# Optimization experiments

Measured on AMD Instinct MI355X. Metric: run time of the kernel, lower is better.

Reference implementation:

```python
import jax, jax.numpy as jnp
import numpy as np
from jax import lax

D_MODEL = 512
N_LAYERS = 12
D_STATE = 16
D_INNER = 2 * D_MODEL          # expand=2
DT_RANK = D_MODEL // 16        # 32
D_CONV = 4
L = 361                        # 19x19 Go board
B = 64


def silu(v):
    return v * jax.nn.sigmoid(v)


def setup_inputs() -> dict:
    key = jax.random.key(0)
    ks = jax.random.split(key, 24)
    s = 0.02
    inp = {
        "x": jax.random.normal(ks[0], (B, 17, 19, 19), dtype=jnp.float32),
        "conv1_w": jax.random.normal(ks[1], (D_MODEL // 4, 17, 3, 3)) * s,
        "conv1_b": jnp.zeros((D_MODEL // 4,)),
        "conv2_w": jax.random.normal(ks[2], (D_MODEL, D_MODEL // 4, 1, 1)) * s,
        "conv2_b": jnp.zeros((D_MODEL,)),
        "spatial_link": jax.random.normal(ks[3], (L, D_MODEL)) * s,
        # stacked per-layer Mamba parameters (leading dim = N_LAYERS)
        "in_proj_w": jax.random.normal(ks[4], (N_LAYERS, 2 * D_INNER, D_MODEL)) * s,
        "conv1d_w": jax.random.normal(ks[5], (N_LAYERS, D_INNER, D_CONV)) * 0.1,
        "conv1d_b": jnp.zeros((N_LAYERS, D_INNER)),
        "x_proj_w": jax.random.normal(ks[6], (N_LAYERS, DT_RANK + 2 * D_STATE, D_INNER)) * s,
        "dt_proj_w": jax.random.normal(ks[7], (N_LAYERS, D_INNER, DT_RANK)) * 0.1,
        "dt_proj_b": jax.random.uniform(ks[8], (N_LAYERS, D_INNER), minval=-4.0, maxval=-2.0),
        "A_log": jnp.broadcast_to(jnp.log(jnp.arange(1.0, D_STATE + 1.0)), (N_LAYERS, D_INNER, D_STATE)) * jnp.ones((N_LAYERS, D_INNER, 1)),
        "D_skip": jnp.ones((N_LAYERS, D_INNER)),
        "out_proj_w": jax.random.normal(ks[9], (N_LAYERS, D_MODEL, D_INNER)) * s,
        "ln_g": jnp.ones((D_MODEL,)),
        "ln_b": jnp.zeros((D_MODEL,)),
        "policy_w": jax.random.normal(ks[10], (362, D_MODEL)) * s,
        "policy_b": jnp.zeros((362,)),
        "value_w": jax.random.normal(ks[11], (1, D_MODEL)) * s,
        "value_b": jnp.zeros((1,)),
    }
    return inp


def _mamba_block(u, p):
    """One Mamba block. u: [B, L, d_model]; p: per-layer params."""
    ipw, cw, cb, xpw, dpw, dpb, alog, dsk, opw = p
    Lh = u.shape[1]
    xz = jnp.einsum('bld,ed->ble', u, ipw)           # [B,L,2*d_inner]
    xc, z = jnp.split(xz, 2, axis=-1)
    # depthwise causal conv1d (kernel 4, left pad 3)
    xp = jnp.pad(xc, ((0, 0), (D_CONV - 1, 0), (0, 0)))
    xc = sum(xp[:, k:k + Lh, :] * cw[:, k] for k in range(D_CONV)) + cb
    xc = silu(xc)
    dbc = jnp.einsum('bld,ed->ble', xc, xpw)          # [B,L,dt_rank+2N]
    dt_r = dbc[..., :DT_RANK]
    Bc = dbc[..., DT_RANK:DT_RANK + D_STATE]
    Cc = dbc[..., DT_RANK + D_STATE:]
    dt = jax.nn.softplus(jnp.einsum('blr,dr->bld', dt_r, dpw) + dpb)  # [B,L,d_inner]
    A = -jnp.exp(alog)                                # [d_inner, N]

    def step(h, xs_t):
        dt_t, B_t, C_t, u_t = xs_t                    # [B,d_inner],[B,N],[B,N],[B,d_inner]
        dA = jnp.exp(dt_t[:, :, None] * A)            # [B,d_inner,N]
        h = dA * h + (dt_t * u_t)[:, :, None] * B_t[:, None, :]
        y = jnp.einsum('bdn,bn->bd', h, C_t)
        return h, y

    h0 = jnp.zeros((u.shape[0], D_INNER, D_STATE), dtype=u.dtype)
    xs = (dt.transpose(1, 0, 2), Bc.transpose(1, 0, 2),
          Cc.transpose(1, 0, 2), xc.transpose(1, 0, 2))
    _, ys = lax.scan(step, h0, xs)                    # ys: [L,B,d_inner]
    y = ys.transpose(1, 0, 2) + xc * dsk
    y = y * silu(z)
    return jnp.einsum('bld,ed->ble', y, opw)


def reference(x, conv1_w, conv1_b, conv2_w, conv2_b, spatial_link,
              in_proj_w, conv1d_w, conv1d_b, x_proj_w, dt_proj_w, dt_proj_b,
              A_log, D_skip, out_proj_w, ln_g, ln_b,
              policy_w, policy_b, value_w, value_b):
    dn = ('NCHW', 'OIHW', 'NCHW')
    h = lax.conv_general_dilated(x, conv1_w, (1, 1), 'SAME', dimension_numbers=dn)
    h = silu(h + conv1_b[None, :, None, None])
    h = lax.conv_general_dilated(h, conv2_w, (1, 1), 'SAME', dimension_numbers=dn)
    h = h + conv2_b[None, :, None, None]
    b = h.shape[0]
    u = h.reshape(b, D_MODEL, L).transpose(0, 2, 1) + spatial_link  # [B,L,d_model]

    def layer(carry, p):
        return carry + _mamba_block(carry, p), None

    u, _ = lax.scan(layer, u, (in_proj_w, conv1d_w, conv1d_b, x_proj_w,
                               dt_proj_w, dt_proj_b, A_log, D_skip, out_proj_w))

    mu = u.mean(-1, keepdims=True)
    var = ((u - mu) ** 2).mean(-1, keepdims=True)
    un = (u - mu) / jnp.sqrt(var + 1e-5) * ln_g + ln_b
    xg = un.mean(axis=1)                               # [B,d_model]
    policy = xg @ policy_w.T + policy_b                # [B,362]
    value = jnp.tanh(xg @ value_w.T + value_b)         # [B,1]
    return policy, value
```

## Files before the change

kernel.cpp:

```cpp
#include <hip/hip_runtime.h>
#include <hip/hip_bf16.h>
#include <cstdint>

typedef unsigned int  uint32;
typedef unsigned short u16;
typedef __attribute__((ext_vector_type(8))) __bf16  bf16x8;
typedef __attribute__((ext_vector_type(4))) float   f32x4;
typedef __attribute__((ext_vector_type(4))) uint32  u32x4;
typedef __attribute__((ext_vector_type(4))) u16     u16x4;

constexpr int BB = 64;
constexpr int LL = 361;
constexpr int DM = 512;
constexpr int DI = 1024;
constexpr int MM = BB * LL;
constexpr int MP = 23168;
constexpr int POL_OUT = BB * 362;

constexpr size_t SCRATCH_BYTES = 700ull * 1024 * 1024;
__device__ __attribute__((aligned(256))) char g_scratch[SCRATCH_BYTES];

__device__ __forceinline__ uint32 bf_rne(float x) {
  uint32 u = __float_as_uint(x);
  return (u + 0x7FFFu + ((u >> 16) & 1u)) >> 16;
}
__device__ __forceinline__ void split2(float v, u16& h, u16& l) {
  uint32 b = __float_as_uint(v);
  h = (u16)(b >> 16);
  l = (u16)bf_rne(v - __uint_as_float(b & 0xFFFF0000u));
}
__device__ __forceinline__ float join2(u16 h, u16 l) {
  return __uint_as_float((uint32)h << 16) + __uint_as_float((uint32)l << 16);
}

template<int ROWS>
__device__ __forceinline__ void stage_swz(const u16* __restrict__ plane, int row0,
                                          int K, int k0, u16* lds,
                                          int wave, int lane) {
  const int lrow = lane >> 3, lslot = lane & 7;
  constexpr int RPW = ROWS / 4;
#pragma unroll
  for (int i = 0; i < RPW / 8; ++i) {
    int rr = wave * RPW + i * 8 + lrow;
    int sg = lslot ^ (rr & 7);
    const u16* src = plane + (size_t)(row0 + rr) * K + k0 + sg * 8;
    u16* dst = lds + (wave * RPW + i * 8) * 64;
    __builtin_amdgcn_global_load_lds(
        (const __attribute__((address_space(1))) void*)src,
        (__attribute__((address_space(3))) void*)dst, 16, 0, 0);
  }
}

template<int BM, int BN, bool RES, bool WPL>
__global__ __launch_bounds__(256, 2) void gemm_pl(
    const u16* __restrict__ Ahi, const u16* __restrict__ Alo,
    const u16* __restrict__ Whi, const u16* __restrict__ Wlo,
    float* __restrict__ C, u16* __restrict__ Chi, u16* __restrict__ Clo,
    int M, int K, int ldc)
{
  constexpr int BK = 64;
  __shared__ __attribute__((aligned(16))) u16 sAh[BM * 64];
  __shared__ __attribute__((aligned(16))) u16 sAl[BM * 64];
  __shared__ __attribute__((aligned(16))) u16 sWh[BN * 64];
  __shared__ __attribute__((aligned(16))) u16 sWl[BN * 64];
  const int tid = threadIdx.x;
  const int m0 = blockIdx.x * BM;
  const int n0 = blockIdx.y * BN;
  const int wave = tid >> 6, lane = tid & 63;
  const int wm = (wave >> 1) * (BM / 2);
  const int wn = (wave & 1) * (BN / 2);
  constexpr int FM = BM / 32, FN = BN / 32;
  f32x4 acc[FM][FN];
#pragma unroll
  for (int i = 0; i < FM; ++i)
#pragma unroll
    for (int j = 0; j < FN; ++j) acc[i][j] = f32x4{0.f, 0.f, 0.f, 0.f};
  const int lr = lane & 15, lq = lane >> 4;

  for (int k0 = 0; k0 < K; k0 += BK) {
    __syncthreads();
    stage_swz<BM>(Ahi, m0, K, k0, sAh, wave, lane);
    stage_swz<BM>(Alo, m0, K, k0, sAl, wave, lane);
    stage_swz<BN>(Whi, n0, K, k0, sWh, wave, lane);
    stage_swz<BN>(Wlo, n0, K, k0, sWl, wave, lane);
    __syncthreads();
#pragma unroll
    for (int kk = 0; kk < 2; ++kk) {
      bf16x8 ah[FM], al[FM], bh[FN], bl[FN];
#pragma unroll
      for (int f = 0; f < FM; ++f) {
        int row = wm + f * 16 + lr;
        int off = row * 128 + (((kk * 4 + lq) ^ (row & 7)) << 4);
        ah[f] = *(const bf16x8*)((const char*)sAh + off);
        al[f] = *(const bf16x8*)((const char*)sAl + off);
      }
#pragma unroll
      for (int f = 0; f < FN; ++f) {
        int row = wn + f * 16 + lr;
        int off = row * 128 + (((kk * 4 + lq) ^ (row & 7)) << 4);
        bh[f] = *(const bf16x8*)((const char*)sWh + off);
        bl[f] = *(const bf16x8*)((const char*)sWl + off);
      }
#pragma unroll
      for (int i = 0; i < FM; ++i)
#pragma unroll
        for (int j = 0; j < FN; ++j) {
          acc[i][j] = __builtin_amdgcn_mfma_f32_16x16x32_bf16(ah[i], bh[j], acc[i][j], 0, 0, 0);
          acc[i][j] = __builtin_amdgcn_mfma_f32_16x16x32_bf16(ah[i], bl[j], acc[i][j], 0, 0, 0);
          acc[i][j] = __builtin_amdgcn_mfma_f32_16x16x32_bf16(al[i], bh[j], acc[i][j], 0, 0, 0);
        }
    }
  }
#pragma unroll
  for (int i = 0; i < FM; ++i)
#pragma unroll
    for (int j = 0; j < FN; ++j) {
      int col = n0 + wn + j * 16 + lr;
#pragma unroll
      for (int q = 0; q < 4; ++q) {
        int row = m0 + wm + i * 16 + lq * 4 + q;
        if (row < M) {
          size_t idx = (size_t)row * ldc + col;
          float v = acc[i][j][q];
          if (RES) v += C[idx];
          C[idx] = v;
          if (WPL) { u16 h, l; split2(v, h, l); Chi[idx] = h; Clo[idx] = l; }
        }
      }
    }
}

__global__ void wconv_kernel(const float* __restrict__ w, u16* __restrict__ hi,
                             u16* __restrict__ lo, int n4) {
  int i = blockIdx.x * 256 + threadIdx.x;
  if (i >= n4) return;
  f32x4 v = *(const f32x4*)&w[(size_t)i * 4];
  u16x4 hv, lv;
#pragma unroll
  for (int q = 0; q < 4; ++q) { u16 h, l; split2(v[q], h, l); hv[q] = h; lv[q] = l; }
  *(u16x4*)&hi[(size_t)i * 4] = hv;
  *(u16x4*)&lo[(size_t)i * 4] = lv;
}

__global__ void w2t_kernel(const float* __restrict__ w2, float* __restrict__ w2t) {
  int i = blockIdx.x * 256 + threadIdx.x;
  if (i < 512 * 128) { int co = i >> 7, ci = i & 127; w2t[ci * 512 + co] = w2[i]; }
}

__global__ void pwt_kernel(const float* __restrict__ pw, float* __restrict__ pwt) {
  int i = blockIdx.x * 256 + threadIdx.x;
  if (i < 362 * 512) { int j = i / 512, dd = i & 511; pwt[dd * 362 + j] = pw[i]; }
}

__global__ void conv1_kernel(const float* __restrict__ x, const float* __restrict__ w,
                             const float* __restrict__ bias, float* __restrict__ h1) {
  __shared__ float xs[17 * 361];
  __shared__ float wls[16 * 153];
  const int b = blockIdx.x, cg = blockIdx.y * 16;
  const int tid = threadIdx.x;
  for (int i = tid; i < 17 * 361; i += 384) xs[i] = x[(size_t)b * 17 * 361 + i];
  for (int i = tid; i < 16 * 153; i += 384) wls[i] = w[(size_t)cg * 153 + i];
  __syncthreads();
  if (tid >= 361) return;
  const int py = tid / 19, px = tid % 19;
  float* outp = h1 + ((size_t)b * 361 + tid) * 128 + cg;
  for (int c = 0; c < 16; ++c) {
    float acc = bias[cg + c];
    const float* wc = wls + c * 153;
    for (int ci = 0; ci < 17; ++ci) {
      const float* xi = xs + ci * 361;
      const float* wi = wc + ci * 9;
#pragma unroll
      for (int ky = 0; ky < 3; ++ky) {
        int iy = py + ky - 1;
        if (iy < 0 || iy >= 19) continue;
#pragma unroll
        for (int kx = 0; kx < 3; ++kx) {
          int ix = px + kx - 1;
          if (ix < 0 || ix >= 19) continue;
          acc += xi[iy * 19 + ix] * wi[ky * 3 + kx];
        }
      }
    }
    outp[c] = acc / (1.f + __expf(-acc));
  }
}

__global__ void conv2_kernel(const float* __restrict__ h1, const float* __restrict__ w2t,
                             const float* __restrict__ b2, const float* __restrict__ sl,
                             float* __restrict__ u, u16* __restrict__ uhi,
                             u16* __restrict__ ulo) {
  __shared__ float hs[8][128];
  const int b = blockIdx.x, l0 = blockIdx.y * 8;
  const int nl = min(8, 361 - l0);
  const int tid = threadIdx.x;
  for (int i = tid; i < nl * 128; i += 512)
    hs[i >> 7][i & 127] = h1[((size_t)b * 361 + l0 + (i >> 7)) * 128 + (i & 127)];
  __syncthreads();
  float acc[8];
#pragma unroll
  for (int j = 0; j < 8; ++j) acc[j] = 0.f;
  for (int ci = 0; ci < 128; ++ci) {
    float wv = w2t[ci * 512 + tid];
#pragma unroll
    for (int j = 0; j < 8; ++j) acc[j] += hs[j][ci] * wv;
  }
  float bb = b2[tid];
  for (int j = 0; j < nl; ++j) {
    int l = l0 + j;
    size_t idx = ((size_t)b * 361 + l) * 512 + tid;
    float v = acc[j] + bb + sl[(size_t)l * 512 + tid];
    u[idx] = v;
    u16 h, lo; split2(v, h, lo);
    uhi[idx] = h; ulo[idx] = lo;
  }
}

__global__ void conv1d_kernel(const float* __restrict__ xz, const float* __restrict__ cw,
                              const float* __restrict__ cb, u16* __restrict__ xchi,
                              u16* __restrict__ xclo) {
  const int b = blockIdx.x, l0 = blockIdx.y * 32;
  const int d = threadIdx.x * 4;
  float w[4][4], bias[4];
#pragma unroll
  for (int j = 0; j < 4; ++j) {
#pragma unroll
    for (int k = 0; k < 4; ++k) w[j][k] = cw[(d + j) * 4 + k];
    bias[j] = cb[d + j];
  }
  f32x4 h0 = {0, 0, 0, 0}, h1v = {0, 0, 0, 0}, h2v = {0, 0, 0, 0};
  if (l0 >= 3) h0  = *(const f32x4*)&xz[((size_t)b * 361 + l0 - 3) * 2048 + d];
  if (l0 >= 2) h1v = *(const f32x4*)&xz[((size_t)b * 361 + l0 - 2) * 2048 + d];
  if (l0 >= 1) h2v = *(const f32x4*)&xz[((size_t)b * 361 + l0 - 1) * 2048 + d];
  const int nl = min(32, 361 - l0);
  for (int t = 0; t < nl; ++t) {
    const int l = l0 + t;
    f32x4 cur = *(const f32x4*)&xz[((size_t)b * 361 + l) * 2048 + d];
    u16x4 hv, lv;
#pragma unroll
    for (int j = 0; j < 4; ++j) {
      float v = h0[j] * w[j][0] + h1v[j] * w[j][1] + h2v[j] * w[j][2] + cur[j] * w[j][3] + bias[j];
      v = v / (1.f + __expf(-v));
      u16 h, lo; split2(v, h, lo); hv[j] = h; lv[j] = lo;
    }
    size_t idx = ((size_t)b * 361 + l) * 1024 + d;
    *(u16x4*)&xchi[idx] = hv;
    *(u16x4*)&xclo[idx] = lv;
    h0 = h1v; h1v = h2v; h2v = cur;
  }
}

__global__ void dt_kernel(const float* __restrict__ dbc, const float* __restrict__ dpw,
                          const float* __restrict__ dpb, float* __restrict__ dty) {
  __shared__ float dbs[32][32];
  const int m0 = blockIdx.x * 32, d0 = blockIdx.y * 256;
  const int tid = threadIdx.x;
  {
    int r = tid >> 3, c = (tid & 7) * 4;
    *(f32x4*)&dbs[r][c] = *(const f32x4*)&dbc[(size_t)(m0 + r) * 64 + c];
  }
  __syncthreads();
  float wreg[32];
  const float* wp = dpw + (size_t)(d0 + tid) * 32;
#pragma unroll
  for (int q = 0; q < 8; ++q) {
    f32x4 v = *(const f32x4*)&wp[q * 4];
    wreg[q * 4] = v[0]; wreg[q * 4 + 1] = v[1]; wreg[q * 4 + 2] = v[2]; wreg[q * 4 + 3] = v[3];
  }
  const float bias = dpb[d0 + tid];
  for (int m = 0; m < 32; ++m) {
    float acc = bias;
#pragma unroll
    for (int r = 0; r < 32; ++r) acc += dbs[m][r] * wreg[r];
    float sp = fmaxf(acc, 0.f) + log1pf(__expf(-fabsf(acc)));
    dty[(size_t)(m0 + m) * 1024 + d0 + tid] = sp;
  }
}

__global__ void scan_kernel(const float* __restrict__ dbc, const u16* __restrict__ xchi,
                            const u16* __restrict__ xclo, const float* __restrict__ xz,
                            const float* __restrict__ alog, const float* __restrict__ dsk,
                            const float* __restrict__ dty, u16* __restrict__ yhi,
                            u16* __restrict__ ylo) {
  const int b = blockIdx.x;
  const int d = blockIdx.y * 256 + threadIdx.x;
  float Ax[16], h[16];
#pragma unroll
  for (int n = 0; n < 16; ++n) { Ax[n] = -__expf(alog[(size_t)d * 16 + n]); h[n] = 0.f; }
  const float dval = dsk[d];
  const size_t mb = (size_t)b * 361;
  for (int t = 0; t < 361; ++t) {
    const size_t m = mb + t;
    const float dtv = dty[m * 1024 + d];
    const float uv  = join2(xchi[m * 1024 + d], xclo[m * 1024 + d]);
    const float zv  = xz[m * 2048 + 1024 + d];
    const float* bcp = dbc + m * 64 + 32;
    const float du = dtv * uv;
    float yv = 0.f;
#pragma unroll
    for (int n = 0; n < 16; ++n) {
      float dA = __expf(dtv * Ax[n]);
      h[n] = dA * h[n] + du * bcp[n];
      yv += h[n] * bcp[16 + n];
    }
    yv += uv * dval;
    float sz = zv / (1.f + __expf(-zv));
    float yo = yv * sz;
    u16 hh, ll; split2(yo, hh, ll);
    yhi[m * 1024 + d] = hh;
    ylo[m * 1024 + d] = ll;
  }
}

__global__ void ln_stats_kernel(const float* __restrict__ u, float* __restrict__ muv,
                                float* __restrict__ rsd) {
  const int m = blockIdx.x * 4 + (threadIdx.x >> 6);
  const int lane = threadIdx.x & 63;
  const float* row = u + (size_t)m * 512;
  float s = 0.f, s2 = 0.f;
#pragma unroll
  for (int i = 0; i < 2; ++i) {
    f32x4 v = *(const f32x4*)&row[(lane + i * 64) * 4];
    s  += v[0] + v[1] + v[2] + v[3];
    s2 += v[0] * v[0] + v[1] * v[1] + v[2] * v[2] + v[3] * v[3];
  }
#pragma unroll
  for (int o = 32; o > 0; o >>= 1) { s += __shfl_down(s, o); s2 += __shfl_down(s2, o); }
  if (lane == 0) {
    float mean = s * (1.f / 512.f);
    float var = s2 * (1.f / 512.f) - mean * mean;
    muv[m] = mean;
    rsd[m] = rsqrtf(var + 1e-5f);
  }
}

__global__ void xg_kernel(const float* __restrict__ u, const float* __restrict__ muv,
                          const float* __restrict__ rsd, const float* __restrict__ g,
                          const float* __restrict__ bta, float* __restrict__ xg) {
  const int b = blockIdx.x, dd = threadIdx.x;
  float acc = 0.f;
  const size_t mb = (size_t)b * 361;
  for (int l = 0; l < 361; ++l) {
    const size_t m = mb + l;
    acc += (u[m * 512 + dd] - muv[m]) * rsd[m];
  }
  xg[(size_t)b * 512 + dd] = g[dd] * acc * (1.f / 361.f) + bta[dd];
}

__global__ void head_kernel(const float* __restrict__ xg, const float* __restrict__ pwt,
                            const float* __restrict__ pb, const float* __restrict__ vw,
                            const float* __restrict__ vb, float* __restrict__ out) {
  __shared__ float xs[512];
  const int b = blockIdx.x, tid = threadIdx.x;
  xs[tid] = xg[(size_t)b * 512 + tid];
  __syncthreads();
  if (tid < 362) {
    float acc = pb[tid];
    for (int dd = 0; dd < 512; ++dd) acc += xs[dd] * pwt[dd * 362 + tid];
    out[(size_t)b * 362 + tid] = acc;
  } else if (tid == 384) {
    float acc = vb[0];
    for (int dd = 0; dd < 512; ++dd) acc += xs[dd] * vw[dd];
    out[POL_OUT + b] = tanhf(acc);
  }
}

extern "C" void kernel_launch(void* const* d_in, const int* in_sizes, int n_in,
                              void* d_out, int out_size, void* d_ws, size_t ws_size,
                              hipStream_t stream) {
  const float* x     = (const float*)d_in[0];
  const float* c1w   = (const float*)d_in[1];
  const float* c1b   = (const float*)d_in[2];
  const float* c2w   = (const float*)d_in[3];
  const float* c2b   = (const float*)d_in[4];
  const float* slink = (const float*)d_in[5];
  const float* ipw   = (const float*)d_in[6];
  const float* cdw   = (const float*)d_in[7];
  const float* cdb   = (const float*)d_in[8];
  const float* xpw   = (const float*)d_in[9];
  const float* dpw   = (const float*)d_in[10];
  const float* dpb   = (const float*)d_in[11];
  const float* alog  = (const float*)d_in[12];
  const float* dskp  = (const float*)d_in[13];
  const float* opw   = (const float*)d_in[14];
  const float* lng   = (const float*)d_in[15];
  const float* lnb   = (const float*)d_in[16];
  const float* pw    = (const float*)d_in[17];
  const float* pb    = (const float*)d_in[18];
  const float* vw    = (const float*)d_in[19];
  const float* vb    = (const float*)d_in[20];
  float* out = (float*)d_out;
  (void)in_sizes; (void)n_in; (void)out_size; (void)d_ws; (void)ws_size;

  char* base = nullptr;
  hipGetSymbolAddress((void**)&base, HIP_SYMBOL(g_scratch));
  size_t off = 0;
  auto carve = [&](size_t bytes) -> char* {
    char* p = base + off;
    off += (bytes + 255) & ~(size_t)255;
    return p;
  };
  float* u    = (float*)carve((size_t)MM * DM * 4);
  float* xz   = (float*)carve((size_t)MM * 2 * DI * 4);
  float* dty  = (float*)carve((size_t)MM * DI * 4);
  float* dbc  = (float*)carve((size_t)MM * 64 * 4);
  float* h1   = (float*)carve((size_t)BB * LL * 128 * 4);
  float* w2t  = (float*)carve(512 * 128 * 4);
  float* pwt  = (float*)carve(512 * 362 * 4);
  float* muv  = (float*)carve((size_t)MM * 4);
  float* rsd  = (float*)carve((size_t)MM * 4);
  float* xg   = (float*)carve((size_t)BB * DM * 4);
  u16* uhi  = (u16*)carve((size_t)MP * DM * 2);
  u16* ulo  = (u16*)carve((size_t)MP * DM * 2);
  u16* xchi = (u16*)carve((size_t)MP * DI * 2);
  u16* xclo = (u16*)carve((size_t)MP * DI * 2);
  u16* yhi  = (u16*)carve((size_t)MP * DI * 2);
  u16* ylo  = (u16*)carve((size_t)MP * DI * 2);
  u16* wih = (u16*)carve((size_t)12 * 2048 * 512 * 2);
  u16* wil = (u16*)carve((size_t)12 * 2048 * 512 * 2);
  u16* wxh = (u16*)carve((size_t)12 * 64 * 1024 * 2);
  u16* wxl = (u16*)carve((size_t)12 * 64 * 1024 * 2);
  u16* woh = (u16*)carve((size_t)12 * 512 * 1024 * 2);
  u16* wol = (u16*)carve((size_t)12 * 512 * 1024 * 2);

  wconv_kernel<<<dim3(12288), dim3(256), 0, stream>>>(ipw, wih, wil, 3145728);
  wconv_kernel<<<dim3(768),   dim3(256), 0, stream>>>(xpw, wxh, wxl, 196608);
  wconv_kernel<<<dim3(6144),  dim3(256), 0, stream>>>(opw, woh, wol, 1572864);
  w2t_kernel<<<dim3(256), dim3(256), 0, stream>>>(c2w, w2t);
  pwt_kernel<<<dim3(724), dim3(256), 0, stream>>>(pw, pwt);

  conv1_kernel<<<dim3(64, 8),  dim3(384), 0, stream>>>(x, c1w, c1b, h1);
  conv2_kernel<<<dim3(64, 46), dim3(512), 0, stream>>>(h1, w2t, c2b, slink, u, uhi, ulo);

  for (int layer = 0; layer < 12; ++layer) {
    gemm_pl<128, 128, false, false><<<dim3(181, 16), dim3(256), 0, stream>>>(
        uhi, ulo, wih + (size_t)layer * 1048576, wil + (size_t)layer * 1048576,
        xz, nullptr, nullptr, MM, 512, 2048);
    conv1d_kernel<<<dim3(64, 12), dim3(256), 0, stream>>>(
        xz, cdw + (size_t)layer * 4096, cdb + (size_t)layer * 1024, xchi, xclo);
    gemm_pl<64, 64, false, false><<<dim3(362, 1), dim3(256), 0, stream>>>(
        xchi, xclo, wxh + (size_t)layer * 65536, wxl + (size_t)layer * 65536,
        dbc, nullptr, nullptr, MM, 1024, 64);
    dt_kernel<<<dim3(722, 4), dim3(256), 0, stream>>>(
        dbc, dpw + (size_t)layer * 32768, dpb + (size_t)layer * 1024, dty);
    scan_kernel<<<dim3(64, 4), dim3(256), 0, stream>>>(
        dbc, xchi, xclo, xz, alog + (size_t)layer * 16384, dskp + (size_t)layer * 1024,
        dty, yhi, ylo);
    gemm_pl<128, 128, true, true><<<dim3(181, 4), dim3(256), 0, stream>>>(
        yhi, ylo, woh + (size_t)layer * 524288, wol + (size_t)layer * 524288,
        u, uhi, ulo, MM, 1024, 512);
  }

  ln_stats_kernel<<<dim3(5776), dim3(256), 0, stream>>>(u, muv, rsd);
  xg_kernel<<<dim3(64), dim3(512), 0, stream>>>(u, muv, rsd, lng, lnb, xg);
  head_kernel<<<dim3(64), dim3(512), 0, stream>>>(xg, pwt, pb, vw, vb, out);
}
```

Measured before the change: 9.205 ms.

## Split scan state across four lanes and add XCD-aware GEMM tile swizzle

The selective scan now assigns four threads per channel, each holding four of the sixteen state elements. Partial outputs are combined with lane shuffles, and loads for the next timestep are software-pipelined, so the grid grows fourfold and occupancy rises on what was an under-filled, latency-bound kernel. GEMM launches become 1D with a remap that gives each XCD a contiguous range of tiles, meant to improve L2 reuse. The costs are redundant per-lane loads of dt, u and z, plus the shuffle overhead.

New measurement: 9.120 ms. No clear change (-0.9%).

```diff
diff --git a/kernel.cpp b/kernel.cpp
--- a/kernel.cpp
+++ b/kernel.cpp
@@ -51,7 +51,7 @@
   }
 }
 
-template<int BM, int BN, bool RES, bool WPL>
+template<int BM, int BN, int GY, bool RES, bool WPL>
 __global__ __launch_bounds__(256, 2) void gemm_pl(
     const u16* __restrict__ Ahi, const u16* __restrict__ Alo,
     const u16* __restrict__ Whi, const u16* __restrict__ Wlo,
@@ -64,8 +64,13 @@
   __shared__ __attribute__((aligned(16))) u16 sWh[BN * 64];
   __shared__ __attribute__((aligned(16))) u16 sWl[BN * 64];
   const int tid = threadIdx.x;
-  const int m0 = blockIdx.x * BM;
-  const int n0 = blockIdx.y * BN;
+  const int nwg = gridDim.x;
+  const int wgid = blockIdx.x;
+  const int q = nwg >> 3, r = nwg & 7;
+  const int xcd = wgid & 7, kk0 = wgid >> 3;
+  const int swz = (xcd < r ? xcd * (q + 1) : r * (q + 1) + (xcd - r) * q) + kk0;
+  const int m0 = (swz / GY) * BM;
+  const int n0 = (swz % GY) * BN;
   const int wave = tid >> 6, lane = tid & 63;
   const int wm = (wave >> 1) * (BM / 2);
   const int wn = (wave & 1) * (BN / 2);
@@ -117,11 +122,11 @@
     for (int j = 0; j < FN; ++j) {
       int col = n0 + wn + j * 16 + lr;
 #pragma unroll
-      for (int q = 0; q < 4; ++q) {
-        int row = m0 + wm + i * 16 + lq * 4 + q;
+      for (int q2 = 0; q2 < 4; ++q2) {
+        int row = m0 + wm + i * 16 + lq * 4 + q2;
         if (row < M) {
           size_t idx = (size_t)row * ldc + col;
-          float v = acc[i][j][q];
+          float v = acc[i][j][q2];
           if (RES) v += C[idx];
           C[idx] = v;
           if (WPL) { u16 h, l; split2(v, h, l); Chi[idx] = h; Clo[idx] = l; }
@@ -277,39 +282,63 @@
   }
 }
 
-__global__ void scan_kernel(const float* __restrict__ dbc, const u16* __restrict__ xchi,
-                            const u16* __restrict__ xclo, const float* __restrict__ xz,
-                            const float* __restrict__ alog, const float* __restrict__ dsk,
-                            const float* __restrict__ dty, u16* __restrict__ yhi,
-                            u16* __restrict__ ylo) {
+__global__ __launch_bounds__(256, 4) void scan_kernel(
+    const float* __restrict__ dbc, const u16* __restrict__ xchi,
+    const u16* __restrict__ xclo, const float* __restrict__ xz,
+    const float* __restrict__ alog, const float* __restrict__ dsk,
+    const float* __restrict__ dty, u16* __restrict__ yhi, u16* __restrict__ ylo) {
   const int b = blockIdx.x;
-  const int d = blockIdx.y * 256 + threadIdx.x;
-  float Ax[16], h[16];
-#pragma unroll
-  for (int n = 0; n < 16; ++n) { Ax[n] = -__expf(alog[(size_t)d * 16 + n]); h[n] = 0.f; }
+  const int tid = threadIdx.x;
+  const int dl = tid >> 2, sg = tid & 3;
+  const int d = blockIdx.y * 64 + dl;
+  const int n0 = sg * 4;
+  float Ax[4], h[4];
+  for (int n = 0; n < 4; ++n) {
+    Ax[n] = -__expf(alog[(size_t)d * 16 + n0 + n]);
+    h[n] = 0.f;
+  }
   const float dval = dsk[d];
   const size_t mb = (size_t)b * 361;
-  for (int t = 0; t < 361; ++t) {
-    const size_t m = mb + t;
-    const float dtv = dty[m * 1024 + d];
-    const float uv  = join2(xchi[m * 1024 + d], xclo[m * 1024 + d]);
-    const float zv  = xz[m * 2048 + 1024 + d];
-    const float* bcp = dbc + m * 64 + 32;
-    const float du = dtv * uv;
-    float yv = 0.f;
-#pragma unroll
-    for (int n = 0; n < 16; ++n) {
-      float dA = __expf(dtv * Ax[n]);
-      h[n] = dA * h[n] + du * bcp[n];
-      yv += h[n] * bcp[16 + n];
-    }
-    yv += uv * dval;
-    float sz = zv / (1.f + __expf(-zv));
-    float yo = yv * sz;
-    u16 hh, ll; split2(yo, hh, ll);
-    yhi[m * 1024 + d] = hh;
-    ylo[m * 1024 + d] = ll;
-  }
+
+#define SC_LOAD(P) \
+    { size_t m_ = mb + (size_t)(P##_t); \
+      P##_dt = dty[m_ * 1024 + d]; \
+      P##_u  = join2(xchi[m_ * 1024 + d], xclo[m_ * 1024 + d]); \
+      P##_z  = xz[m_ * 2048 + 1024 + d]; \
+      const float* bcp_ = dbc + m_ * 64 + 32 + n0; \
+      P##_B = *(const f32x4*)bcp_; \
+      P##_C = *(const f32x4*)(bcp_ + 16); }
+
+#define SC_COMP(P) \
+    { float du_ = P##_dt * P##_u; \
+      float y_ = 0.f; \
+      for (int n = 0; n < 4; ++n) { \
+        float dA_ = __expf(P##_dt * Ax[n]); \
+        h[n] = dA_ * h[n] + du_ * P##_B[n]; \
+        y_ += h[n] * P##_C[n]; \
+      } \
+      y_ += __shfl_xor(y_, 1); \
+      y_ += __shfl_xor(y_, 2); \
+      y_ += P##_u * dval; \
+      float sz_ = P##_z / (1.f + __expf(-P##_z)); \
+      float yo_ = y_ * sz_; \
+      u16 hh_, ll_; split2(yo_, hh_, ll_); \
+      size_t mo_ = mb + (size_t)(P##_t); \
+      if (sg == 0) yhi[mo_ * 1024 + d] = hh_; \
+      else if (sg == 1) ylo[mo_ * 1024 + d] = ll_; }
+
+  int pa_t; float pa_dt, pa_u, pa_z; f32x4 pa_B, pa_C;
+  int pb_t; float pb_dt, pb_u, pb_z; f32x4 pb_B, pb_C;
+  pa_t = 0; SC_LOAD(pa);
+  for (int t = 0; t + 2 <= 361; t += 2) {
+    pb_t = t + 1; SC_LOAD(pb);
+    SC_COMP(pa);
+    pa_t = t + 2; SC_LOAD(pa);
+    SC_COMP(pb);
+  }
+  SC_COMP(pa);
+#undef SC_LOAD
+#undef SC_COMP
 }
 
 __global__ void ln_stats_kernel(const float* __restrict__ u, float* __restrict__ muv,
@@ -433,20 +462,20 @@
   conv2_kernel<<<dim3(64, 46), dim3(512), 0, stream>>>(h1, w2t, c2b, slink, u, uhi, ulo);
 
   for (int layer = 0; layer < 12; ++layer) {
-    gemm_pl<128, 128, false, false><<<dim3(181, 16), dim3(256), 0, stream>>>(
+    gemm_pl<128, 128, 16, false, false><<<dim3(181 * 16), dim3(256), 0, stream>>>(
         uhi, ulo, wih + (size_t)layer * 1048576, wil + (size_t)layer * 1048576,
         xz, nullptr, nullptr, MM, 512, 2048);
     conv1d_kernel<<<dim3(64, 12), dim3(256), 0, stream>>>(
         xz, cdw + (size_t)layer * 4096, cdb + (size_t)layer * 1024, xchi, xclo);
-    gemm_pl<64, 64, false, false><<<dim3(362, 1), dim3(256), 0, stream>>>(
+    gemm_pl<64, 64, 1, false, false><<<dim3(362), dim3(256), 0, stream>>>(
         xchi, xclo, wxh + (size_t)layer * 65536, wxl + (size_t)layer * 65536,
         dbc, nullptr, nullptr, MM, 1024, 64);
     dt_kernel<<<dim3(722, 4), dim3(256), 0, stream>>>(
         dbc, dpw + (size_t)layer * 32768, dpb + (size_t)layer * 1024, dty);
-    scan_kernel<<<dim3(64, 4), dim3(256), 0, stream>>>(
+    scan_kernel<<<dim3(64, 16), dim3(256), 0, stream>>>(
         dbc, xchi, xclo, xz, alog + (size_t)layer * 16384, dskp + (size_t)layer * 1024,
         dty, yhi, ylo);
-    gemm_pl<128, 128, true, true><<<dim3(181, 4), dim3(256), 0, stream>>>(
+    gemm_pl<128, 128, 4, true, true><<<dim3(181 * 4), dim3(256), 0, stream>>>(
         yhi, ylo, woh + (size_t)layer * 524288, wol + (size_t)layer * 524288,
         u, uhi, ulo, MM, 1024, 512);
   }
```
